# Kernel tuning notes

Hardware: AMD Instinct MI355X
Metric: run time of the kernel (lower is better)

The kernel has to match this reference:

```python
import jax, jax.numpy as jnp
import numpy as np

N = 8192          # number of atoms
N_ELEM = 95       # r2r4 table size (elements 0..94)
EPS = 1e-12


def setup_inputs() -> dict:
    key = jax.random.key(0)
    k1, k2, k3 = jax.random.split(key, 3)
    atomic_numbers = jax.random.randint(k1, (N,), 0, N_ELEM)
    # positions in a ~60 Angstrom box so pair distances are realistic
    positions = jax.random.uniform(k2, (N, 3), dtype=jnp.float32) * 60.0
    r2r4 = jax.random.uniform(k3, (N_ELEM,), dtype=jnp.float32)
    # Becke-Johnson damping parameters (PBE D3-BJ)
    a1 = jnp.float32(0.4289)
    a2 = jnp.float32(4.4407)
    s6 = jnp.float32(1.0)
    s8 = jnp.float32(0.7875)
    return {"atomic_numbers": atomic_numbers, "positions": positions,
            "r2r4": r2r4, "a1": a1, "a2": a2, "s6": s6, "s8": s8}


def reference(atomic_numbers, positions, r2r4, a1, a2, s6, s8):
    # Per-atom-type gather (present in source; mathematically unused because
    # the source hard-codes c6 = c8 = 1 via all-ones LazyTensors).
    r2r4_z = r2r4[atomic_numbers]                      # (N,)

    # All-pairs squared distances. d appears only as d^6 and d^8, which are
    # polynomials in d2, so no sqrt is needed (also keeps diagonal smooth).
    diff = positions[:, None, :] - positions[None, :, :]   # (N, N, 3)
    d2 = jnp.sum(diff * diff, axis=-1)                     # (N, N)
    d6 = d2 * d2 * d2
    d8 = d6 * d2

    # c6 = c8 = 1  =>  tmp = a1 * sqrt(c8/c6) + a2 = a1 + a2
    tmp = a1 + a2
    tmp2 = tmp * tmp
    tmp6 = tmp2 * tmp2 * tmp2
    tmp8 = tmp6 * tmp2

    c6 = jnp.float32(1.0)
    c8 = jnp.float32(1.0)
    D_ij = -s6 * c6 / (d6 + tmp6 + EPS) - s8 * c8 / (d8 + tmp8 + EPS)

    # mask d > eps  <=>  d2 > eps^2 (removes self-terms)
    mask = d2 > EPS * EPS
    D_ij = jnp.where(mask, D_ij, jnp.float32(0.0))

    # a_i = sum_j D_ij ; energy = sum_i a_i
    return jnp.sum(D_ij) + jnp.float32(0.0) * jnp.sum(r2r4_z)
```

## Files before the change

### kernel.cpp

```cpp
#include <hip/hip_runtime.h>

#define NA 8192
#define TILE 128
#define NT (NA / TILE)
#define NBLK (NT * (NT + 1) / 2)
#define NSPLIT 4
#define BLOCK (TILE * NSPLIT)
#define JPT (TILE / NSPLIT)
#define S_OF(r) ((r) * NT - (r) * ((r) - 1) / 2)

__global__ __launch_bounds__(BLOCK, 8) void dftd3_pair_energy(
    const float* __restrict__ pos,
    const float* __restrict__ p_a1, const float* __restrict__ p_a2,
    const float* __restrict__ p_s6, const float* __restrict__ p_s8,
    float* __restrict__ out)
{
    const int b = blockIdx.x;
    int ti = (int)((2 * NT + 1 - sqrtf((float)((2 * NT + 1) * (2 * NT + 1) - 8 * b))) * 0.5f);
    if (ti > NT - 1) ti = NT - 1;
    if (ti < 0) ti = 0;
    while (S_OF(ti + 1) <= b) ++ti;
    while (S_OF(ti) > b) --ti;
    const int tj = ti + (b - S_OF(ti));

    __shared__ float4 sj[TILE];
    __shared__ float wsum[BLOCK / 64];

    const int tid  = threadIdx.x;
    const int li   = tid & (TILE - 1);
    const int part = tid >> 7;

    if (tid < TILE) {
        const int j = tj * TILE + tid;
        sj[tid] = make_float4(pos[3 * j + 0], pos[3 * j + 1], pos[3 * j + 2], 0.0f);
    }

    const int i = ti * TILE + li;
    const float xi = pos[3 * i + 0];
    const float yi = pos[3 * i + 1];
    const float zi = pos[3 * i + 2];

    const float a1 = p_a1[0], a2 = p_a2[0];
    const float s6 = p_s6[0], s8 = p_s8[0];
    const float tmp  = a1 + a2;
    const float tmp2 = tmp * tmp;
    const float tmp6 = tmp2 * tmp2 * tmp2;
    const float tmp8 = tmp6 * tmp2;
    const float T6 = tmp6 + 1e-12f;
    const float T8 = tmp8 + 1e-12f;
    const float ns6 = -s6, ns8 = -s8;
    const float EPS2 = 1e-24f;

    __syncthreads();

    float acc0 = 0.0f, acc1 = 0.0f;
    const int j0 = part * JPT;

    auto body = [&](int k, bool masked) {
        float4 p = sj[j0 + k];
        float dx = xi - p.x;
        float dy = yi - p.y;
        float dz = zi - p.z;
        float d2 = fmaf(dx, dx, fmaf(dy, dy, dz * dz));
        float d4 = d2 * d2;
        float d6 = d4 * d2;
        float d8 = d4 * d4;
        float A  = d6 + T6;
        float B  = d8 + T8;
        float num = fmaf(ns6, B, ns8 * A);
        if (masked) num = (d2 > EPS2) ? num : 0.0f;
        float r = __builtin_amdgcn_rcpf(A * B);
        if (k & 1) acc1 = fmaf(num, r, acc1);
        else       acc0 = fmaf(num, r, acc0);
    };

    if (ti == tj) {
        #pragma unroll 16
        for (int k = 0; k < JPT; ++k) body(k, true);
    } else {
        #pragma unroll 16
        for (int k = 0; k < JPT; ++k) body(k, false);
    }

    float acc = acc0 + acc1;
    if (ti != tj) acc *= 2.0f;

    #pragma unroll
    for (int off = 32; off > 0; off >>= 1)
        acc += __shfl_xor(acc, off, 64);

    if ((tid & 63) == 0) wsum[tid >> 6] = acc;
    __syncthreads();
    if (tid == 0) {
        float s = 0.0f;
        #pragma unroll
        for (int w = 0; w < BLOCK / 64; ++w) s += wsum[w];
        atomicAdd(out, s);
    }
}

extern "C" void kernel_launch(void* const* d_in, const int* in_sizes, int n_in,
                              void* d_out, int out_size, void* d_ws, size_t ws_size,
                              hipStream_t stream) {
    const float* pos = (const float*)d_in[1];
    const float* a1  = (const float*)d_in[3];
    const float* a2  = (const float*)d_in[4];
    const float* s6  = (const float*)d_in[5];
    const float* s8  = (const float*)d_in[6];
    float* out = (float*)d_out;

    hipMemsetAsync(out, 0, sizeof(float), stream);

    dftd3_pair_energy<<<dim3(NBLK), BLOCK, 0, stream>>>(pos, a1, a2, s6, s8, out);
}
```

Measured before the change: 101.5 us.

## Read j-positions via uniform scalar loads and spread atomics across slots

Removes the shared-memory staging of j-tile positions and the first barrier. Each wave instead reads j positions directly from global memory through a wave-uniform pointer (readfirstlane on the part index), so the compiler can use scalar loads. The single global atomic is replaced by 16 partial slots in workspace plus a tiny reduction kernel, which cuts atomic contention but adds a second launch. The unroll factor drops from 16 to 8.

```diff
diff --git a/kernel.cpp b/kernel.cpp
--- a/kernel.cpp
+++ b/kernel.cpp
@@ -7,13 +7,14 @@
 #define NSPLIT 4
 #define BLOCK (TILE * NSPLIT)
 #define JPT (TILE / NSPLIT)
+#define NSLOT 16
 #define S_OF(r) ((r) * NT - (r) * ((r) - 1) / 2)
 
 __global__ __launch_bounds__(BLOCK, 8) void dftd3_pair_energy(
     const float* __restrict__ pos,
     const float* __restrict__ p_a1, const float* __restrict__ p_a2,
     const float* __restrict__ p_s6, const float* __restrict__ p_s8,
-    float* __restrict__ out)
+    float* __restrict__ partial)
 {
     const int b = blockIdx.x;
     int ti = (int)((2 * NT + 1 - sqrtf((float)((2 * NT + 1) * (2 * NT + 1) - 8 * b))) * 0.5f);
@@ -23,17 +24,9 @@
     while (S_OF(ti) > b) --ti;
     const int tj = ti + (b - S_OF(ti));
 
-    __shared__ float4 sj[TILE];
-    __shared__ float wsum[BLOCK / 64];
-
     const int tid  = threadIdx.x;
     const int li   = tid & (TILE - 1);
-    const int part = tid >> 7;
-
-    if (tid < TILE) {
-        const int j = tj * TILE + tid;
-        sj[tid] = make_float4(pos[3 * j + 0], pos[3 * j + 1], pos[3 * j + 2], 0.0f);
-    }
+    const int part = __builtin_amdgcn_readfirstlane(tid >> 7);
 
     const int i = ti * TILE + li;
     const float xi = pos[3 * i + 0];
@@ -51,16 +44,17 @@
     const float ns6 = -s6, ns8 = -s8;
     const float EPS2 = 1e-24f;
 
-    __syncthreads();
+    const float* __restrict__ pj = pos + 3 * (tj * TILE + part * JPT);
 
     float acc0 = 0.0f, acc1 = 0.0f;
-    const int j0 = part * JPT;
 
     auto body = [&](int k, bool masked) {
-        float4 p = sj[j0 + k];
-        float dx = xi - p.x;
-        float dy = yi - p.y;
-        float dz = zi - p.z;
+        float px = pj[3 * k + 0];
+        float py = pj[3 * k + 1];
+        float pz = pj[3 * k + 2];
+        float dx = xi - px;
+        float dy = yi - py;
+        float dz = zi - pz;
         float d2 = fmaf(dx, dx, fmaf(dy, dy, dz * dz));
         float d4 = d2 * d2;
         float d6 = d4 * d2;
@@ -75,10 +69,10 @@
     };
 
     if (ti == tj) {
-        #pragma unroll 16
+        #pragma unroll 8
         for (int k = 0; k < JPT; ++k) body(k, true);
     } else {
-        #pragma unroll 16
+        #pragma unroll 8
         for (int k = 0; k < JPT; ++k) body(k, false);
     }
 
@@ -89,13 +83,24 @@
     for (int off = 32; off > 0; off >>= 1)
         acc += __shfl_xor(acc, off, 64);
 
+    __shared__ float wsum[BLOCK / 64];
     if ((tid & 63) == 0) wsum[tid >> 6] = acc;
     __syncthreads();
     if (tid == 0) {
         float s = 0.0f;
         #pragma unroll
         for (int w = 0; w < BLOCK / 64; ++w) s += wsum[w];
-        atomicAdd(out, s);
+        atomicAdd(&partial[b & (NSLOT - 1)], s);
+    }
+}
+
+__global__ void reduce_slots(const float* __restrict__ partial, float* __restrict__ out)
+{
+    if (threadIdx.x == 0) {
+        float s = 0.0f;
+        #pragma unroll
+        for (int k = 0; k < NSLOT; ++k) s += partial[k];
+        out[0] = s;
     }
 }
 
@@ -107,9 +112,11 @@
     const float* a2  = (const float*)d_in[4];
     const float* s6  = (const float*)d_in[5];
     const float* s8  = (const float*)d_in[6];
+    float* partial = (float*)d_ws;
     float* out = (float*)d_out;
 
-    hipMemsetAsync(out, 0, sizeof(float), stream);
+    hipMemsetAsync(partial, 0, NSLOT * sizeof(float), stream);
 
-    dftd3_pair_energy<<<dim3(NBLK), BLOCK, 0, stream>>>(pos, a1, a2, s6, s8, out);
+    dftd3_pair_energy<<<dim3(NBLK), BLOCK, 0, stream>>>(pos, a1, a2, s6, s8, partial);
+    reduce_slots<<<1, 64, 0, stream>>>(partial, out);
 }
```

Measured after the change: 95.07 us. -6.4%, faster.
